# Kernel optimization log

Hardware: AMD Instinct MI355X
Metric: run time of the kernel (lower is better)

Reference implementation:

```python
import jax, jax.numpy as jnp
import numpy as np

TOP_K = 8  # num_experts_per_tok


def setup_inputs() -> dict:
    key = jax.random.key(0)
    k1, k2, k3 = jax.random.split(key, 3)
    B, S, H, E = 4, 4096, 2048, 64
    hidden_states = jax.random.normal(k1, (B, S, H), dtype=jnp.float32)
    router_weight = jax.random.normal(k2, (E, H), dtype=jnp.float32)
    router_bias = jnp.zeros((E,), dtype=jnp.float32)
    expert_bias = jax.random.normal(k3, (E, H), dtype=jnp.float32) * 0.1
    return {
        "hidden_states": hidden_states,
        "router_weight": router_weight,
        "router_bias": router_bias,
        "expert_bias": expert_bias,
    }


def reference(hidden_states, router_weight, router_bias, expert_bias):
    B, S, H = hidden_states.shape
    flat = hidden_states.reshape(B * S, H)  # [T, H]
    # Router: linear -> softmax -> top-k
    logits = jnp.einsum("th,eh->te", flat, router_weight) + router_bias
    scores = jax.nn.softmax(logits, axis=-1)
    topk_w, topk_idx = jax.lax.top_k(scores, TOP_K)  # [T, K]
    # Dispatch/combine collapses to: combined[t,k] = x[t] + expert_bias[idx[t,k]]
    # output[t] = sum_k w[t,k] * combined[t,k]
    #          = x[t] * sum_k w[t,k] + sum_k w[t,k] * expert_bias[idx[t,k]]
    gathered_bias = expert_bias[topk_idx]  # [T, K, H]
    out = flat * jnp.sum(topk_w, axis=-1, keepdims=True) + jnp.einsum(
        "tk,tkh->th", topk_w, gathered_bias
    )
    return out.reshape(B, S, H)
```

## Files before the change

kernel.cpp:

```cpp
#include <hip/hip_runtime.h>
#include <hip/hip_bf16.h>
#include <float.h>

#define H 2048
#define E 64
#define TOPK 8
#define TT 16

typedef __attribute__((ext_vector_type(8))) short bf16x8;
typedef __attribute__((ext_vector_type(4))) float f32x4;
typedef __attribute__((ext_vector_type(4))) unsigned short us4;

__device__ __forceinline__ unsigned short f2bf(float f) {
  unsigned u = __float_as_uint(f);
  u += 0x7fffu + ((u >> 16) & 1u);
  return (unsigned short)(u >> 16);
}
__device__ __forceinline__ float bf2f(unsigned short s) {
  return __uint_as_float(((unsigned)s) << 16);
}
__device__ __forceinline__ float wred_max(float v) {
#pragma unroll
  for (int o = 32; o > 0; o >>= 1) v = fmaxf(v, __shfl_xor(v, o));
  return v;
}
__device__ __forceinline__ float wred_sum(float v) {
#pragma unroll
  for (int o = 32; o > 0; o >>= 1) v += __shfl_xor(v, o);
  return v;
}

__global__ __launch_bounds__(256) void cvt_kernel(const float* __restrict__ W,
                                                  const float* __restrict__ eb,
                                                  unsigned short* __restrict__ Wb,
                                                  unsigned short* __restrict__ Bb) {
  int i = (blockIdx.x * 256 + threadIdx.x) * 4;
  const float* src;
  unsigned short* dst;
  int off;
  if (i < E * H) { src = W; dst = Wb; off = i; }
  else           { src = eb; dst = Bb; off = i - E * H; }
  float4 v = *(const float4*)(src + off);
  us4 r;
  r[0] = f2bf(v.x); r[1] = f2bf(v.y); r[2] = f2bf(v.z); r[3] = f2bf(v.w);
  *(us4*)(dst + off) = r;
}

template <bool USE_WS>
__global__ __launch_bounds__(256, 2) void moe_kernel(
    const float* __restrict__ x, const float* __restrict__ W,
    const float* __restrict__ rb, const float* __restrict__ eb,
    const unsigned short* __restrict__ Wb, const unsigned short* __restrict__ Bb,
    float* __restrict__ out) {
  __shared__ unsigned short xl[TT][H + 8];
  __shared__ float lg[TT][E + 1];
  __shared__ float msw[TT];
  __shared__ float mw[TT][TOPK];
  __shared__ int   mi[TT][TOPK];

  const int tid = threadIdx.x;
  const int t0  = blockIdx.x * TT;

  {
    const int c0 = tid * 4;
#pragma unroll 4
    for (int j = 0; j < TT; ++j) {
      const float* row = x + (size_t)(t0 + j) * H;
      float4 a = *(const float4*)(row + c0);
      float4 b = *(const float4*)(row + 1024 + c0);
      us4 ra, rbv;
      ra[0] = f2bf(a.x); ra[1] = f2bf(a.y); ra[2] = f2bf(a.z); ra[3] = f2bf(a.w);
      rbv[0] = f2bf(b.x); rbv[1] = f2bf(b.y); rbv[2] = f2bf(b.z); rbv[3] = f2bf(b.w);
      *(us4*)&xl[j][c0] = ra;
      *(us4*)&xl[j][1024 + c0] = rbv;
    }
  }
  __syncthreads();

  const int wv = tid >> 6, lane = tid & 63, quad = lane >> 4, m = lane & 15;

  {
    const int e = wv * 16 + m;
    f32x4 acc = {0.f, 0.f, 0.f, 0.f};
    const unsigned short* xp = &xl[m][quad * 8];
    if (USE_WS) {
      const unsigned short* wp = Wb + (size_t)e * H + quad * 8;
#pragma unroll 8
      for (int it = 0; it < H / 32; ++it) {
        bf16x8 av = *(const bf16x8*)(xp + it * 32);
        bf16x8 bv = *(const bf16x8*)(wp + it * 32);
        acc = __builtin_amdgcn_mfma_f32_16x16x32_bf16(av, bv, acc, 0, 0, 0);
      }
    } else {
      const float* wp = W + (size_t)e * H + quad * 8;
#pragma unroll 4
      for (int it = 0; it < H / 32; ++it) {
        bf16x8 av = *(const bf16x8*)(xp + it * 32);
        float4 p = *(const float4*)(wp + it * 32);
        float4 q = *(const float4*)(wp + it * 32 + 4);
        bf16x8 bv;
        bv[0] = (short)f2bf(p.x); bv[1] = (short)f2bf(p.y);
        bv[2] = (short)f2bf(p.z); bv[3] = (short)f2bf(p.w);
        bv[4] = (short)f2bf(q.x); bv[5] = (short)f2bf(q.y);
        bv[6] = (short)f2bf(q.z); bv[7] = (short)f2bf(q.w);
        acc = __builtin_amdgcn_mfma_f32_16x16x32_bf16(av, bv, acc, 0, 0, 0);
      }
    }
#pragma unroll
    for (int r = 0; r < 4; ++r) lg[quad * 4 + r][wv * 16 + m] = acc[r];
  }
  __syncthreads();

  {
#pragma unroll
    for (int tt = 0; tt < 4; ++tt) {
      const int t = wv * 4 + tt;
      float l = lg[t][lane] + rb[lane];
      const float mx = wred_max(l);
      const float p = expf(l - mx);
      const float inv = 1.f / wred_sum(p);
      float sumw = 0.f;
      float lsel = l;
#pragma unroll
      for (int k = 0; k < TOPK; ++k) {
        const float mk = wred_max(lsel);
        const unsigned long long b = __ballot(lsel == mk);
        const int idx = __ffsll(b) - 1;
        const float wk = expf(mk - mx) * inv;
        sumw += wk;
        if (lane == 0) { mw[t][k] = wk; mi[t][k] = idx; }
        if (lane == idx) lsel = -FLT_MAX;
      }
      if (lane == 0) msw[t] = sumw;
    }
  }
  __syncthreads();

  {
    const int c = tid * 8;
    for (int t = 0; t < TT; ++t) {
      const float sw = msw[t];
      bf16x8 xv = *(const bf16x8*)&xl[t][c];
      float o[8];
#pragma unroll
      for (int i = 0; i < 8; ++i) o[i] = bf2f((unsigned short)xv[i]) * sw;
#pragma unroll
      for (int k = 0; k < TOPK; ++k) {
        const int e = mi[t][k];
        const float wk = mw[t][k];
        if (USE_WS) {
          bf16x8 bvv = *(const bf16x8*)(Bb + (size_t)e * H + c);
#pragma unroll
          for (int i = 0; i < 8; ++i) o[i] += wk * bf2f((unsigned short)bvv[i]);
        } else {
          float4 p = *(const float4*)(eb + (size_t)e * H + c);
          float4 q = *(const float4*)(eb + (size_t)e * H + c + 4);
          o[0] += wk * p.x; o[1] += wk * p.y; o[2] += wk * p.z; o[3] += wk * p.w;
          o[4] += wk * q.x; o[5] += wk * q.y; o[6] += wk * q.z; o[7] += wk * q.w;
        }
      }
      float* orow = out + (size_t)(t0 + t) * H + c;
      *(float4*)orow       = make_float4(o[0], o[1], o[2], o[3]);
      *(float4*)(orow + 4) = make_float4(o[4], o[5], o[6], o[7]);
    }
  }
}

extern "C" void kernel_launch(void* const* d_in, const int* in_sizes, int n_in,
                              void* d_out, int out_size, void* d_ws, size_t ws_size,
                              hipStream_t stream) {
  const float* x  = (const float*)d_in[0];
  const float* W  = (const float*)d_in[1];
  const float* rb = (const float*)d_in[2];
  const float* eb = (const float*)d_in[3];
  float* out = (float*)d_out;

  const int T = in_sizes[0] / H;
  const int grid = T / TT;

  const size_t need = (size_t)2 * E * H * sizeof(unsigned short);
  if (ws_size >= need) {
    unsigned short* Wb = (unsigned short*)d_ws;
    unsigned short* Bb = Wb + E * H;
    cvt_kernel<<<(2 * E * H) / (256 * 4), 256, 0, stream>>>(W, eb, Wb, Bb);
    moe_kernel<true><<<grid, 256, 0, stream>>>(x, W, rb, eb, Wb, Bb, out);
  } else {
    moe_kernel<false><<<grid, 256, 0, stream>>>(x, W, rb, eb, nullptr, nullptr, out);
  }
}
```

Before: 298.0 us.

## Drop LDS staging of activations and raise occupancy to four blocks per CU

Removes the shared-memory bf16 copy of the token tile and has each wave load and convert x directly from global memory in the router GEMM and again in fp32 for the combine step. Freeing roughly 64KB of LDS per block lets launch bounds request four blocks per CU for better latency hiding. In exchange x is fetched several times per block from global/L2 instead of once, and conversion work is repeated per wave.

```diff
diff --git a/kernel.cpp b/kernel.cpp
--- a/kernel.cpp
+++ b/kernel.cpp
@@ -6,6 +6,7 @@
 #define E 64
 #define TOPK 8
 #define TT 16
+#define NT 256
 
 typedef __attribute__((ext_vector_type(8))) short bf16x8;
 typedef __attribute__((ext_vector_type(4))) float f32x4;
@@ -47,12 +48,11 @@
 }
 
 template <bool USE_WS>
-__global__ __launch_bounds__(256, 2) void moe_kernel(
+__global__ __launch_bounds__(NT, 4) void moe_kernel(
     const float* __restrict__ x, const float* __restrict__ W,
     const float* __restrict__ rb, const float* __restrict__ eb,
     const unsigned short* __restrict__ Wb, const unsigned short* __restrict__ Bb,
     float* __restrict__ out) {
-  __shared__ unsigned short xl[TT][H + 8];
   __shared__ float lg[TT][E + 1];
   __shared__ float msw[TT];
   __shared__ float mw[TT][TOPK];
@@ -60,49 +60,44 @@
 
   const int tid = threadIdx.x;
   const int t0  = blockIdx.x * TT;
-
-  {
-    const int c0 = tid * 4;
-#pragma unroll 4
-    for (int j = 0; j < TT; ++j) {
-      const float* row = x + (size_t)(t0 + j) * H;
-      float4 a = *(const float4*)(row + c0);
-      float4 b = *(const float4*)(row + 1024 + c0);
-      us4 ra, rbv;
-      ra[0] = f2bf(a.x); ra[1] = f2bf(a.y); ra[2] = f2bf(a.z); ra[3] = f2bf(a.w);
-      rbv[0] = f2bf(b.x); rbv[1] = f2bf(b.y); rbv[2] = f2bf(b.z); rbv[3] = f2bf(b.w);
-      *(us4*)&xl[j][c0] = ra;
-      *(us4*)&xl[j][1024 + c0] = rbv;
-    }
-  }
-  __syncthreads();
-
   const int wv = tid >> 6, lane = tid & 63, quad = lane >> 4, m = lane & 15;
 
   {
     const int e = wv * 16 + m;
     f32x4 acc = {0.f, 0.f, 0.f, 0.f};
-    const unsigned short* xp = &xl[m][quad * 8];
+    const float* xp = x + (size_t)(t0 + m) * H + quad * 8;
     if (USE_WS) {
       const unsigned short* wp = Wb + (size_t)e * H + quad * 8;
-#pragma unroll 8
+#pragma unroll 4
       for (int it = 0; it < H / 32; ++it) {
-        bf16x8 av = *(const bf16x8*)(xp + it * 32);
+        float4 p = *(const float4*)(xp + it * 32);
+        float4 q = *(const float4*)(xp + it * 32 + 4);
+        bf16x8 av;
+        av[0] = (short)f2bf(p.x); av[1] = (short)f2bf(p.y);
+        av[2] = (short)f2bf(p.z); av[3] = (short)f2bf(p.w);
+        av[4] = (short)f2bf(q.x); av[5] = (short)f2bf(q.y);
+        av[6] = (short)f2bf(q.z); av[7] = (short)f2bf(q.w);
         bf16x8 bv = *(const bf16x8*)(wp + it * 32);
         acc = __builtin_amdgcn_mfma_f32_16x16x32_bf16(av, bv, acc, 0, 0, 0);
       }
     } else {
       const float* wp = W + (size_t)e * H + quad * 8;
-#pragma unroll 4
+#pragma unroll 2
       for (int it = 0; it < H / 32; ++it) {
-        bf16x8 av = *(const bf16x8*)(xp + it * 32);
-        float4 p = *(const float4*)(wp + it * 32);
-        float4 q = *(const float4*)(wp + it * 32 + 4);
+        float4 p = *(const float4*)(xp + it * 32);
+        float4 q = *(const float4*)(xp + it * 32 + 4);
+        bf16x8 av;
+        av[0] = (short)f2bf(p.x); av[1] = (short)f2bf(p.y);
+        av[2] = (short)f2bf(p.z); av[3] = (short)f2bf(p.w);
+        av[4] = (short)f2bf(q.x); av[5] = (short)f2bf(q.y);
+        av[6] = (short)f2bf(q.z); av[7] = (short)f2bf(q.w);
+        float4 wp0 = *(const float4*)(wp + it * 32);
+        float4 wq0 = *(const float4*)(wp + it * 32 + 4);
         bf16x8 bv;
-        bv[0] = (short)f2bf(p.x); bv[1] = (short)f2bf(p.y);
-        bv[2] = (short)f2bf(p.z); bv[3] = (short)f2bf(p.w);
-        bv[4] = (short)f2bf(q.x); bv[5] = (short)f2bf(q.y);
-        bv[6] = (short)f2bf(q.z); bv[7] = (short)f2bf(q.w);
+        bv[0] = (short)f2bf(wp0.x); bv[1] = (short)f2bf(wp0.y);
+        bv[2] = (short)f2bf(wp0.z); bv[3] = (short)f2bf(wp0.w);
+        bv[4] = (short)f2bf(wq0.x); bv[5] = (short)f2bf(wq0.y);
+        bv[6] = (short)f2bf(wq0.z); bv[7] = (short)f2bf(wq0.w);
         acc = __builtin_amdgcn_mfma_f32_16x16x32_bf16(av, bv, acc, 0, 0, 0);
       }
     }
@@ -140,18 +135,19 @@
     const int c = tid * 8;
     for (int t = 0; t < TT; ++t) {
       const float sw = msw[t];
-      bf16x8 xv = *(const bf16x8*)&xl[t][c];
-      float o[8];
-#pragma unroll
-      for (int i = 0; i < 8; ++i) o[i] = bf2f((unsigned short)xv[i]) * sw;
+      const float* xrow = x + (size_t)(t0 + t) * H + c;
+      float4 xa = *(const float4*)xrow;
+      float4 xb = *(const float4*)(xrow + 4);
+      float o[8] = {xa.x * sw, xa.y * sw, xa.z * sw, xa.w * sw,
+                    xb.x * sw, xb.y * sw, xb.z * sw, xb.w * sw};
 #pragma unroll
       for (int k = 0; k < TOPK; ++k) {
         const int e = mi[t][k];
         const float wk = mw[t][k];
         if (USE_WS) {
-          bf16x8 bvv = *(const bf16x8*)(Bb + (size_t)e * H + c);
+          bf16x8 bv = *(const bf16x8*)(Bb + (size_t)e * H + c);
 #pragma unroll
-          for (int i = 0; i < 8; ++i) o[i] += wk * bf2f((unsigned short)bvv[i]);
+          for (int i = 0; i < 8; ++i) o[i] += wk * bf2f((unsigned short)bv[i]);
         } else {
           float4 p = *(const float4*)(eb + (size_t)e * H + c);
           float4 q = *(const float4*)(eb + (size_t)e * H + c + 4);
@@ -183,8 +179,8 @@
     unsigned short* Wb = (unsigned short*)d_ws;
     unsigned short* Bb = Wb + E * H;
     cvt_kernel<<<(2 * E * H) / (256 * 4), 256, 0, stream>>>(W, eb, Wb, Bb);
-    moe_kernel<true><<<grid, 256, 0, stream>>>(x, W, rb, eb, Wb, Bb, out);
+    moe_kernel<true><<<grid, NT, 0, stream>>>(x, W, rb, eb, Wb, Bb, out);
   } else {
-    moe_kernel<false><<<grid, 256, 0, stream>>>(x, W, rb, eb, nullptr, nullptr, out);
+    moe_kernel<false><<<grid, NT, 0, stream>>>(x, W, rb, eb, nullptr, nullptr, out);
   }
 }
```

Measured after the change: 314.2 us. +5.4%, slower.
